# Kernel optimization log

Hardware: AMD Instinct MI355X
Metric: run time of the kernel (lower is better)

The kernel has to match this reference:

```python
import jax, jax.numpy as jnp
import numpy as np
import math


def _build_lookup(S):
    # Vectorized port of build_hierarchical_index_lookup_table (static, numpy).
    L = int(math.log2(S))
    total = 2 * S - 1
    max_valid = total - 2  # root is never a neighbor
    idx = np.full((S, L), -1, dtype=np.int32)
    cmask = np.zeros((S, L), dtype=bool)
    n = np.arange(S, dtype=np.int64)
    for lvl in range(L):
        if lvl == 0:
            nn = n ^ 1
            pair = n
        else:
            pair = n // 2 + S
            nn = pair ^ 1
        valid = nn <= max_valid
        idx[:, lvl] = np.where(valid, nn.astype(np.int32), idx[:, lvl])
        cmask[:, lvl] = np.where(valid, (pair < nn) & valid, cmask[:, lvl])
        n = nn
    return jnp.asarray(idx), jnp.asarray(cmask)


def _tree_kv(k, v, levels, scale):
    # Build parent nodes bottom-up. Parent K is the mean of its two children;
    # parent V is refined by the fused parent-self attention (build_parent_nodes):
    # 3-way softmax over [self, child0, child1] with eps 1e-9 in the denominator.
    K_parts, V_parts = [k], [v]
    Kc, Vc = k, v
    for _ in range(levels):
        Kc0, Kc1 = Kc[:, 0::2], Kc[:, 1::2]
        Vc0, Vc1 = Vc[:, 0::2], Vc[:, 1::2]
        Kp = 0.5 * (Kc0 + Kc1)
        Vp = 0.5 * (Vc0 + Vc1)
        s_self = jnp.einsum('bphd,bphd->bph', Kp, Kp) * scale
        s0 = jnp.einsum('bphd,bphd->bph', Kp, Kc0) * scale
        s1 = jnp.einsum('bphd,bphd->bph', Kp, Kc1) * scale
        m = jnp.maximum(s_self, jnp.maximum(s0, s1))
        e_self = jnp.exp(s_self - m)
        e0 = jnp.exp(s0 - m)
        e1 = jnp.exp(s1 - m)
        denom = e_self + e0 + e1 + 1e-9
        Vp = (e_self[..., None] * Vp + e0[..., None] * Vc0 + e1[..., None] * Vc1) / denom[..., None]
        K_parts.append(Kp)
        V_parts.append(Vp)
        Kc, Vc = Kp, Vp
    # Full tree: leaves first, then each parent level -> [B, 2S-1, H, D]
    return jnp.concatenate(K_parts, axis=1), jnp.concatenate(V_parts, axis=1)


def setup_inputs() -> dict:
    key = jax.random.key(0)
    kq, kk, kv = jax.random.split(key, 3)
    B, S, H, D = 4, 4096, 8, 64
    q = jax.random.normal(kq, (B, S, H, D), dtype=jnp.float32)
    k = jax.random.normal(kk, (B, S, H, D), dtype=jnp.float32)
    v = jax.random.normal(kv, (B, S, H, D), dtype=jnp.float32)
    return {'q': q, 'k': k, 'v': v}


def reference(q, k, v):
    B, S, H, D = q.shape
    L = int(math.log2(S))
    scale = 1.0 / math.sqrt(D)
    idx, cmask = _build_lookup(S)          # [S, L] int32, [S, L] bool
    Kf, Vf = _tree_kv(k, v, L, scale)      # [B, 2S-1, H, D]
    kc = Kf[:, idx]                        # [B, S, L, H, D] tree-indexed gather
    vc = Vf[:, idx]
    s_self = jnp.einsum('bshd,bshd->bsh', q, k) * scale
    s_cross = jnp.einsum('bshd,bslhd->bshl', q, kc) * scale
    s_cross = jnp.where(cmask[None, :, None, :], -jnp.inf, s_cross)
    m = jnp.maximum(s_self, jnp.max(s_cross, axis=-1))  # online-softmax max
    e_self = jnp.exp(s_self - m)
    e_cross = jnp.exp(s_cross - m[..., None])
    denom = e_self + jnp.sum(e_cross, axis=-1)
    out = (e_self[..., None] * v + jnp.einsum('bshl,bslhd->bshd', e_cross, vc)) / denom[..., None]
    return out
```

## Files before the change

kernel.cpp:

```cpp
#include <hip/hip_runtime.h>


#define S 4096
#define H 8
#define D 64
#define B 4
#define NBH 32
#define NHI 126
#define SCALE 0.125f

__device__ inline float red16(float x) {
    x += __shfl_xor(x, 1);
    x += __shfl_xor(x, 2);
    x += __shfl_xor(x, 4);
    x += __shfl_xor(x, 8);
    return x;
}

__device__ inline float dot4(const float4 a, const float4 b) {
    return a.x * b.x + a.y * b.y + a.z * b.z + a.w * b.w;
}

__device__ inline void combine(const float4 k0, const float4 k1,
                               const float4 v0, const float4 v1,
                               float4& kp, float4& vp) {
    kp.x = 0.5f * (k0.x + k1.x);
    kp.y = 0.5f * (k0.y + k1.y);
    kp.z = 0.5f * (k0.z + k1.z);
    kp.w = 0.5f * (k0.w + k1.w);
    float pss = red16(dot4(kp, kp)) * SCALE;
    float p0  = red16(dot4(kp, k0)) * SCALE;
    float p1  = red16(dot4(kp, k1)) * SCALE;
    float m  = fmaxf(pss, fmaxf(p0, p1));
    float es = __expf(pss - m), e0 = __expf(p0 - m), e1 = __expf(p1 - m);
    float inv = 1.0f / (es + e0 + e1 + 1e-9f);
    float h = 0.5f * es;
    vp.x = ((h + e0) * v0.x + (h + e1) * v1.x) * inv;
    vp.y = ((h + e0) * v0.y + (h + e1) * v1.y) * inv;
    vp.z = ((h + e0) * v0.z + (h + e1) * v1.z) * inv;
    vp.w = ((h + e0) * v0.w + (h + e1) * v1.w) * inv;
}

__global__ __launch_bounds__(256) void chunk_root(
    const float* __restrict__ k, const float* __restrict__ v,
    float* __restrict__ khi, float* __restrict__ vhi)
{
    __shared__ float lkA[32 * 64], lvA[32 * 64];
    __shared__ float lkB[16 * 64], lvB[16 * 64];
    const int t = threadIdx.x;
    const int sub = t & 15;
    const int pg = t >> 4;
    const int blk = blockIdx.x;
    const int c = blk & 63;
    const int bh = blk >> 6;
    const int b = bh >> 3, h = bh & 7;

#pragma unroll
    for (int r = 0; r < 2; ++r) {
        int j = pg + r * 16;
        int s0 = c * 64 + 2 * j;
        size_t a0 = ((((size_t)b * S + s0) * H + h) * D) + sub * 4;
        float4 k0 = *(const float4*)(k + a0);
        float4 k1 = *(const float4*)(k + a0 + H * D);
        float4 v0 = *(const float4*)(v + a0);
        float4 v1 = *(const float4*)(v + a0 + H * D);
        float4 kp, vp;
        combine(k0, k1, v0, v1, kp, vp);
        *(float4*)(lkA + j * 64 + sub * 4) = kp;
        *(float4*)(lvA + j * 64 + sub * 4) = vp;
    }
    __syncthreads();

    float *sk = lkA, *sv = lvA, *dk = lkB, *dv = lvB;
#pragma unroll
    for (int l = 2; l <= 6; ++l) {
        int np = 64 >> l;
        if (pg < np) {
            int j = pg;
            float4 k0 = *(const float4*)(sk + (2 * j) * 64 + sub * 4);
            float4 k1 = *(const float4*)(sk + (2 * j + 1) * 64 + sub * 4);
            float4 v0 = *(const float4*)(sv + (2 * j) * 64 + sub * 4);
            float4 v1 = *(const float4*)(sv + (2 * j + 1) * 64 + sub * 4);
            float4 kp, vp;
            combine(k0, k1, v0, v1, kp, vp);
            if (l < 6) {
                *(float4*)(dk + j * 64 + sub * 4) = kp;
                *(float4*)(dv + j * 64 + sub * 4) = vp;
            } else {
                size_t g = ((size_t)bh * NHI + c) * 64 + sub * 4;
                *(float4*)(khi + g) = kp;
                *(float4*)(vhi + g) = vp;
            }
        }
        __syncthreads();
        float* tp;
        tp = sk; sk = dk; dk = tp;
        tp = sv; sv = dv; dv = tp;
    }
}

__global__ __launch_bounds__(256) void build_hi(
    float* __restrict__ khi, float* __restrict__ vhi)
{
    __shared__ float lk[NHI * 64], lv[NHI * 64];
    const int t = threadIdx.x;
    const int sub = t & 15;
    const int pg = t >> 4;
    const int bh = blockIdx.x;
    size_t base = (size_t)bh * NHI * 64;

    for (int i = t; i < 1024; i += 256) {
        *(float4*)(lk + i * 4) = *(const float4*)(khi + base + i * 4);
        *(float4*)(lv + i * 4) = *(const float4*)(vhi + base + i * 4);
    }
    __syncthreads();

    int srcOff = 0, dstOff = 64, np = 32;
#pragma unroll
    for (int l = 7; l <= 11; ++l) {
        for (int j = pg; j < np; j += 16) {
            float4 k0 = *(const float4*)(lk + (srcOff + 2 * j) * 64 + sub * 4);
            float4 k1 = *(const float4*)(lk + (srcOff + 2 * j + 1) * 64 + sub * 4);
            float4 v0 = *(const float4*)(lv + (srcOff + 2 * j) * 64 + sub * 4);
            float4 v1 = *(const float4*)(lv + (srcOff + 2 * j + 1) * 64 + sub * 4);
            float4 kp, vp;
            combine(k0, k1, v0, v1, kp, vp);
            *(float4*)(lk + (dstOff + j) * 64 + sub * 4) = kp;
            *(float4*)(lv + (dstOff + j) * 64 + sub * 4) = vp;
            *(float4*)(khi + base + (size_t)(dstOff + j) * 64 + sub * 4) = kp;
            *(float4*)(vhi + base + (size_t)(dstOff + j) * 64 + sub * 4) = vp;
        }
        __syncthreads();
        srcOff = dstOff; dstOff += np; np >>= 1;
    }
}

__global__ __launch_bounds__(256) void attn_chunk(
    const float* __restrict__ q, const float* __restrict__ k,
    const float* __restrict__ v,
    const float* __restrict__ khi, const float* __restrict__ vhi,
    float* __restrict__ out)
{
    __shared__ float tk[62 * 64], tv[62 * 64];
    __shared__ float pk[6 * 64], pv[6 * 64];
    const int t = threadIdx.x;
    const int sub = t & 15;
    const int pg = t >> 4;
    const int blk = blockIdx.x;
    const int c = blk & 63;
    const int bh = blk >> 6;
    const int b = bh >> 3, h = bh & 7;

    if (pg < 12) {
        int lh = (pg >= 6) ? pg - 6 : pg;
        if ((c >> lh) & 1) {
            int off = 128 - (128 >> lh);
            int node = off + ((c >> lh) ^ 1);
            size_t a = ((size_t)bh * NHI + node) * 64 + sub * 4;
            if (pg < 6) *(float4*)(pk + lh * 64 + sub * 4) = *(const float4*)(khi + a);
            else        *(float4*)(pv + lh * 64 + sub * 4) = *(const float4*)(vhi + a);
        }
    }

#pragma unroll
    for (int r = 0; r < 2; ++r) {
        int j = pg + r * 16;
        int s0 = c * 64 + 2 * j;
        size_t a0 = ((((size_t)b * S + s0) * H + h) * D) + sub * 4;
        float4 k0 = *(const float4*)(k + a0);
        float4 k1 = *(const float4*)(k + a0 + H * D);
        float4 v0 = *(const float4*)(v + a0);
        float4 v1 = *(const float4*)(v + a0 + H * D);
        float4 kp, vp;
        combine(k0, k1, v0, v1, kp, vp);
        *(float4*)(tk + j * 64 + sub * 4) = kp;
        *(float4*)(tv + j * 64 + sub * 4) = vp;
    }
    __syncthreads();

    {
        int srcOff = 0, dstOff = 32, np = 16;
#pragma unroll
        for (int l = 2; l <= 5; ++l) {
            if (pg < np) {
                int j = pg;
                float4 k0 = *(const float4*)(tk + (srcOff + 2 * j) * 64 + sub * 4);
                float4 k1 = *(const float4*)(tk + (srcOff + 2 * j + 1) * 64 + sub * 4);
                float4 v0 = *(const float4*)(tv + (srcOff + 2 * j) * 64 + sub * 4);
                float4 v1 = *(const float4*)(tv + (srcOff + 2 * j + 1) * 64 + sub * 4);
                float4 kp, vp;
                combine(k0, k1, v0, v1, kp, vp);
                *(float4*)(tk + (dstOff + j) * 64 + sub * 4) = kp;
                *(float4*)(tv + (dstOff + j) * 64 + sub * 4) = vp;
            }
            __syncthreads();
            srcOff = dstOff; dstOff += np; np >>= 1;
        }
    }

#pragma unroll 1
    for (int r = 0; r < 4; ++r) {
        int sl = pg + r * 16;
        int s = c * 64 + sl;
        size_t qa = ((((size_t)b * S + s) * H + h) * D) + sub * 4;
        float4 q4 = *(const float4*)(q + qa);
        float4 k4 = *(const float4*)(k + qa);
        float4 v4 = *(const float4*)(v + qa);

        float ss = red16(dot4(q4, k4)) * SCALE;

        float sc[12];
        float4 vc0 = v4;
        const bool odd = (s & 1) != 0;
        if (odd) {
            float4 kc0 = *(const float4*)(k + qa - H * D);
            vc0 = *(const float4*)(v + qa - H * D);
            sc[0] = red16(dot4(q4, kc0)) * SCALE;
        } else {
            sc[0] = -1e38f;
        }
#pragma unroll
        for (int l = 1; l <= 5; ++l) {
            if ((s >> l) & 1) {
                int base = 64 - (64 >> (l - 1));
                int loc = base + (((s >> l) ^ 1) - (c << (6 - l)));
                float4 kc = *(const float4*)(tk + loc * 64 + sub * 4);
                sc[l] = red16(dot4(q4, kc)) * SCALE;
            } else sc[l] = -1e38f;
        }
#pragma unroll
        for (int l = 6; l <= 11; ++l) {
            if ((c >> (l - 6)) & 1) {
                float4 kc = *(const float4*)(pk + (l - 6) * 64 + sub * 4);
                sc[l] = red16(dot4(q4, kc)) * SCALE;
            } else sc[l] = -1e38f;
        }

        float m = ss;
#pragma unroll
        for (int l = 0; l < 12; ++l) m = fmaxf(m, sc[l]);

        float es = __expf(ss - m);
        float denom = es;
        float4 acc;
        acc.x = es * v4.x; acc.y = es * v4.y; acc.z = es * v4.z; acc.w = es * v4.w;

        if (odd) {
            float e = __expf(sc[0] - m);
            denom += e;
            acc.x += e * vc0.x; acc.y += e * vc0.y;
            acc.z += e * vc0.z; acc.w += e * vc0.w;
        }
#pragma unroll
        for (int l = 1; l <= 5; ++l) {
            if ((s >> l) & 1) {
                int base = 64 - (64 >> (l - 1));
                int loc = base + (((s >> l) ^ 1) - (c << (6 - l)));
                float4 vc = *(const float4*)(tv + loc * 64 + sub * 4);
                float e = __expf(sc[l] - m);
                denom += e;
                acc.x += e * vc.x; acc.y += e * vc.y;
                acc.z += e * vc.z; acc.w += e * vc.w;
            }
        }
#pragma unroll
        for (int l = 6; l <= 11; ++l) {
            if ((c >> (l - 6)) & 1) {
                float4 vc = *(const float4*)(pv + (l - 6) * 64 + sub * 4);
                float e = __expf(sc[l] - m);
                denom += e;
                acc.x += e * vc.x; acc.y += e * vc.y;
                acc.z += e * vc.z; acc.w += e * vc.w;
            }
        }
        float inv = 1.0f / denom;
        float4 o;
        o.x = acc.x * inv; o.y = acc.y * inv;
        o.z = acc.z * inv; o.w = acc.w * inv;
        *(float4*)(out + qa) = o;
    }
}

extern "C" void kernel_launch(void* const* d_in, const int* in_sizes, int n_in,
                              void* d_out, int out_size, void* d_ws, size_t ws_size,
                              hipStream_t stream) {
    const float* q = (const float*)d_in[0];
    const float* k = (const float*)d_in[1];
    const float* v = (const float*)d_in[2];
    float* outp = (float*)d_out;
    float* khi = (float*)d_ws;
    float* vhi = khi + (size_t)NBH * NHI * D;

    hipLaunchKernelGGL(chunk_root, dim3(NBH * 64), dim3(256), 0, stream,
                       k, v, khi, vhi);
    hipLaunchKernelGGL(build_hi, dim3(NBH), dim3(256), 0, stream, khi, vhi);
    hipLaunchKernelGGL(attn_chunk, dim3(NBH * 64), dim3(256), 0, stream,
                       q, k, v, khi, vhi, outp);
}
```

Before: 168.3 us.

## Fuse upper-tree build into attention kernel, recomputing high levels per block

Removes the separate build_hi kernel, which ran on only 32 blocks. Each attention block now loads all 64 chunk roots for its (b,h) into shared memory and rebuilds the upper tree levels in place, picking up the six sibling nodes it needs into registers. This drops one launch and a low-parallelism serial stage. In exchange each of the 2048 blocks repeats the upper-level reduction, with extra syncs and more shared memory. It also adds launch_bounds occupancy hints and partially unrolls the query loop.

```diff
diff --git a/kernel.cpp b/kernel.cpp
--- a/kernel.cpp
+++ b/kernel.cpp
@@ -6,7 +6,6 @@
 #define D 64
 #define B 4
 #define NBH 32
-#define NHI 126
 #define SCALE 0.125f
 
 __device__ inline float red16(float x) {
@@ -87,7 +86,7 @@
                 *(float4*)(dk + j * 64 + sub * 4) = kp;
                 *(float4*)(dv + j * 64 + sub * 4) = vp;
             } else {
-                size_t g = ((size_t)bh * NHI + c) * 64 + sub * 4;
+                size_t g = ((size_t)bh * 64 + c) * 64 + sub * 4;
                 *(float4*)(khi + g) = kp;
                 *(float4*)(vhi + g) = vp;
             }
@@ -99,50 +98,13 @@
     }
 }
 
-__global__ __launch_bounds__(256) void build_hi(
-    float* __restrict__ khi, float* __restrict__ vhi)
-{
-    __shared__ float lk[NHI * 64], lv[NHI * 64];
-    const int t = threadIdx.x;
-    const int sub = t & 15;
-    const int pg = t >> 4;
-    const int bh = blockIdx.x;
-    size_t base = (size_t)bh * NHI * 64;
-
-    for (int i = t; i < 1024; i += 256) {
-        *(float4*)(lk + i * 4) = *(const float4*)(khi + base + i * 4);
-        *(float4*)(lv + i * 4) = *(const float4*)(vhi + base + i * 4);
-    }
-    __syncthreads();
-
-    int srcOff = 0, dstOff = 64, np = 32;
-#pragma unroll
-    for (int l = 7; l <= 11; ++l) {
-        for (int j = pg; j < np; j += 16) {
-            float4 k0 = *(const float4*)(lk + (srcOff + 2 * j) * 64 + sub * 4);
-            float4 k1 = *(const float4*)(lk + (srcOff + 2 * j + 1) * 64 + sub * 4);
-            float4 v0 = *(const float4*)(lv + (srcOff + 2 * j) * 64 + sub * 4);
-            float4 v1 = *(const float4*)(lv + (srcOff + 2 * j + 1) * 64 + sub * 4);
-            float4 kp, vp;
-            combine(k0, k1, v0, v1, kp, vp);
-            *(float4*)(lk + (dstOff + j) * 64 + sub * 4) = kp;
-            *(float4*)(lv + (dstOff + j) * 64 + sub * 4) = vp;
-            *(float4*)(khi + base + (size_t)(dstOff + j) * 64 + sub * 4) = kp;
-            *(float4*)(vhi + base + (size_t)(dstOff + j) * 64 + sub * 4) = vp;
-        }
-        __syncthreads();
-        srcOff = dstOff; dstOff += np; np >>= 1;
-    }
-}
-
-__global__ __launch_bounds__(256) void attn_chunk(
+__global__ __launch_bounds__(256, 4) void attn_fused(
     const float* __restrict__ q, const float* __restrict__ k,
     const float* __restrict__ v,
     const float* __restrict__ khi, const float* __restrict__ vhi,
     float* __restrict__ out)
 {
-    __shared__ float tk[62 * 64], tv[62 * 64];
-    __shared__ float pk[6 * 64], pv[6 * 64];
+    __shared__ float rk[64 * 64], rv[64 * 64];
     const int t = threadIdx.x;
     const int sub = t & 15;
     const int pg = t >> 4;
@@ -151,15 +113,55 @@
     const int bh = blk >> 6;
     const int b = bh >> 3, h = bh & 7;
 
-    if (pg < 12) {
-        int lh = (pg >= 6) ? pg - 6 : pg;
-        if ((c >> lh) & 1) {
-            int off = 128 - (128 >> lh);
-            int node = off + ((c >> lh) ^ 1);
-            size_t a = ((size_t)bh * NHI + node) * 64 + sub * 4;
-            if (pg < 6) *(float4*)(pk + lh * 64 + sub * 4) = *(const float4*)(khi + a);
-            else        *(float4*)(pv + lh * 64 + sub * 4) = *(const float4*)(vhi + a);
-        }
+    {
+        size_t base = (size_t)bh * 64 * 64;
+        for (int i = t; i < 1024; i += 256) {
+            *(float4*)(rk + i * 4) = *(const float4*)(khi + base + i * 4);
+            *(float4*)(rv + i * 4) = *(const float4*)(vhi + base + i * 4);
+        }
+    }
+    __syncthreads();
+
+    float4 pkr[6], pvr[6];
+    pkr[0] = *(const float4*)(rk + (c ^ 1) * 64 + sub * 4);
+    pvr[0] = *(const float4*)(rv + (c ^ 1) * 64 + sub * 4);
+    __syncthreads();
+
+#pragma unroll
+    for (int tt = 1; tt <= 5; ++tt) {
+        int nc = 64 >> tt;
+        int half = 1 << (tt - 1);
+        if (tt == 1) {
+#pragma unroll
+            for (int r = 0; r < 2; ++r) {
+                int j = pg + r * 16;
+                int r0 = j << 1;
+                float4 k0 = *(const float4*)(rk + r0 * 64 + sub * 4);
+                float4 k1 = *(const float4*)(rk + (r0 + 1) * 64 + sub * 4);
+                float4 v0 = *(const float4*)(rv + r0 * 64 + sub * 4);
+                float4 v1 = *(const float4*)(rv + (r0 + 1) * 64 + sub * 4);
+                float4 kp, vp;
+                combine(k0, k1, v0, v1, kp, vp);
+                *(float4*)(rk + r0 * 64 + sub * 4) = kp;
+                *(float4*)(rv + r0 * 64 + sub * 4) = vp;
+            }
+        } else if (pg < nc) {
+            int r0 = pg << tt;
+            int r1 = r0 + half;
+            float4 k0 = *(const float4*)(rk + r0 * 64 + sub * 4);
+            float4 k1 = *(const float4*)(rk + r1 * 64 + sub * 4);
+            float4 v0 = *(const float4*)(rv + r0 * 64 + sub * 4);
+            float4 v1 = *(const float4*)(rv + r1 * 64 + sub * 4);
+            float4 kp, vp;
+            combine(k0, k1, v0, v1, kp, vp);
+            *(float4*)(rk + r0 * 64 + sub * 4) = kp;
+            *(float4*)(rv + r0 * 64 + sub * 4) = vp;
+        }
+        __syncthreads();
+        int prow = (((c >> tt) ^ 1)) << tt;
+        pkr[tt] = *(const float4*)(rk + prow * 64 + sub * 4);
+        pvr[tt] = *(const float4*)(rv + prow * 64 + sub * 4);
+        __syncthreads();
     }
 
 #pragma unroll
@@ -173,32 +175,31 @@
         float4 v1 = *(const float4*)(v + a0 + H * D);
         float4 kp, vp;
         combine(k0, k1, v0, v1, kp, vp);
-        *(float4*)(tk + j * 64 + sub * 4) = kp;
-        *(float4*)(tv + j * 64 + sub * 4) = vp;
-    }
-    __syncthreads();
-
+        *(float4*)(rk + j * 64 + sub * 4) = kp;
+        *(float4*)(rv + j * 64 + sub * 4) = vp;
+    }
+    __syncthreads();
     {
         int srcOff = 0, dstOff = 32, np = 16;
 #pragma unroll
         for (int l = 2; l <= 5; ++l) {
             if (pg < np) {
                 int j = pg;
-                float4 k0 = *(const float4*)(tk + (srcOff + 2 * j) * 64 + sub * 4);
-                float4 k1 = *(const float4*)(tk + (srcOff + 2 * j + 1) * 64 + sub * 4);
-                float4 v0 = *(const float4*)(tv + (srcOff + 2 * j) * 64 + sub * 4);
-                float4 v1 = *(const float4*)(tv + (srcOff + 2 * j + 1) * 64 + sub * 4);
+                float4 k0 = *(const float4*)(rk + (srcOff + 2 * j) * 64 + sub * 4);
+                float4 k1 = *(const float4*)(rk + (srcOff + 2 * j + 1) * 64 + sub * 4);
+                float4 v0 = *(const float4*)(rv + (srcOff + 2 * j) * 64 + sub * 4);
+                float4 v1 = *(const float4*)(rv + (srcOff + 2 * j + 1) * 64 + sub * 4);
                 float4 kp, vp;
                 combine(k0, k1, v0, v1, kp, vp);
-                *(float4*)(tk + (dstOff + j) * 64 + sub * 4) = kp;
-                *(float4*)(tv + (dstOff + j) * 64 + sub * 4) = vp;
+                *(float4*)(rk + (dstOff + j) * 64 + sub * 4) = kp;
+                *(float4*)(rv + (dstOff + j) * 64 + sub * 4) = vp;
             }
             __syncthreads();
             srcOff = dstOff; dstOff += np; np >>= 1;
         }
     }
 
-#pragma unroll 1
+#pragma unroll 2
     for (int r = 0; r < 4; ++r) {
         int sl = pg + r * 16;
         int s = c * 64 + sl;
@@ -224,15 +225,14 @@
             if ((s >> l) & 1) {
                 int base = 64 - (64 >> (l - 1));
                 int loc = base + (((s >> l) ^ 1) - (c << (6 - l)));
-                float4 kc = *(const float4*)(tk + loc * 64 + sub * 4);
+                float4 kc = *(const float4*)(rk + loc * 64 + sub * 4);
                 sc[l] = red16(dot4(q4, kc)) * SCALE;
             } else sc[l] = -1e38f;
         }
 #pragma unroll
         for (int l = 6; l <= 11; ++l) {
             if ((c >> (l - 6)) & 1) {
-                float4 kc = *(const float4*)(pk + (l - 6) * 64 + sub * 4);
-                sc[l] = red16(dot4(q4, kc)) * SCALE;
+                sc[l] = red16(dot4(q4, pkr[l - 6])) * SCALE;
             } else sc[l] = -1e38f;
         }
 
@@ -256,7 +256,7 @@
             if ((s >> l) & 1) {
                 int base = 64 - (64 >> (l - 1));
                 int loc = base + (((s >> l) ^ 1) - (c << (6 - l)));
-                float4 vc = *(const float4*)(tv + loc * 64 + sub * 4);
+                float4 vc = *(const float4*)(rv + loc * 64 + sub * 4);
                 float e = __expf(sc[l] - m);
                 denom += e;
                 acc.x += e * vc.x; acc.y += e * vc.y;
@@ -266,11 +266,10 @@
 #pragma unroll
         for (int l = 6; l <= 11; ++l) {
             if ((c >> (l - 6)) & 1) {
-                float4 vc = *(const float4*)(pv + (l - 6) * 64 + sub * 4);
                 float e = __expf(sc[l] - m);
                 denom += e;
-                acc.x += e * vc.x; acc.y += e * vc.y;
-                acc.z += e * vc.z; acc.w += e * vc.w;
+                acc.x += e * pvr[l - 6].x; acc.y += e * pvr[l - 6].y;
+                acc.z += e * pvr[l - 6].z; acc.w += e * pvr[l - 6].w;
             }
         }
         float inv = 1.0f / denom;
@@ -289,11 +288,10 @@
     const float* v = (const float*)d_in[2];
     float* outp = (float*)d_out;
     float* khi = (float*)d_ws;
-    float* vhi = khi + (size_t)NBH * NHI * D;
+    float* vhi = khi + (size_t)NBH * 64 * D;
 
     hipLaunchKernelGGL(chunk_root, dim3(NBH * 64), dim3(256), 0, stream,
                        k, v, khi, vhi);
-    hipLaunchKernelGGL(build_hi, dim3(NBH), dim3(256), 0, stream, khi, vhi);
-    hipLaunchKernelGGL(attn_chunk, dim3(NBH * 64), dim3(256), 0, stream,
+    hipLaunchKernelGGL(attn_fused, dim3(NBH * 64), dim3(256), 0, stream,
                        q, k, v, khi, vhi, outp);
 }
```

After: 169.6 us. About the same (+0.7%).

## Shrink attention chunks to 32 tokens and pad shared rows to avoid bank conflicts

Applied to the files above, without the earlier changes.

Reduces the per-block chunk in the attention kernel from 64 to 32 tokens and doubles the grid. Each chunk_root block now builds two 32-token subtrees in place. build_hi now processes 128 chunk roots over 6 levels. Shared-memory rows are padded to 68 floats to reduce LDS bank conflicts, and occupancy hints are added through launch_bounds. The aim is more parallelism and less per-block in-chunk tree work. The cost is more blocks that each redo the leaf-pair combine, plus a larger workspace.

```diff
diff --git a/kernel.cpp b/kernel.cpp
--- a/kernel.cpp
+++ b/kernel.cpp
@@ -6,8 +6,9 @@
 #define D 64
 #define B 4
 #define NBH 32
-#define NHI 126
+#define NHI 254
 #define SCALE 0.125f
+#define ROWF 68
 
 __device__ inline float red16(float x) {
     x += __shfl_xor(x, 1);
@@ -41,24 +42,27 @@
     vp.w = ((h + e0) * v0.w + (h + e1) * v1.w) * inv;
 }
 
-__global__ __launch_bounds__(256) void chunk_root(
+__global__ __launch_bounds__(256, 8) void chunk5(
     const float* __restrict__ k, const float* __restrict__ v,
     float* __restrict__ khi, float* __restrict__ vhi)
 {
-    __shared__ float lkA[32 * 64], lvA[32 * 64];
-    __shared__ float lkB[16 * 64], lvB[16 * 64];
+    __shared__ float lsk[32 * ROWF], lsv[32 * ROWF];
     const int t = threadIdx.x;
     const int sub = t & 15;
     const int pg = t >> 4;
     const int blk = blockIdx.x;
-    const int c = blk & 63;
+    const int pair = blk & 63;
     const int bh = blk >> 6;
     const int b = bh >> 3, h = bh & 7;
+    const int csel = pg >> 3;
+    const int jg = pg & 7;
+    const int c = pair * 2 + csel;
+    const int rowBase = csel * 16;
 
 #pragma unroll
     for (int r = 0; r < 2; ++r) {
-        int j = pg + r * 16;
-        int s0 = c * 64 + 2 * j;
+        int j = jg + r * 8;
+        int s0 = c * 32 + 2 * j;
         size_t a0 = ((((size_t)b * S + s0) * H + h) * D) + sub * 4;
         float4 k0 = *(const float4*)(k + a0);
         float4 k1 = *(const float4*)(k + a0 + H * D);
@@ -66,26 +70,26 @@
         float4 v1 = *(const float4*)(v + a0 + H * D);
         float4 kp, vp;
         combine(k0, k1, v0, v1, kp, vp);
-        *(float4*)(lkA + j * 64 + sub * 4) = kp;
-        *(float4*)(lvA + j * 64 + sub * 4) = vp;
-    }
-    __syncthreads();
-
-    float *sk = lkA, *sv = lvA, *dk = lkB, *dv = lvB;
-#pragma unroll
-    for (int l = 2; l <= 6; ++l) {
-        int np = 64 >> l;
-        if (pg < np) {
-            int j = pg;
-            float4 k0 = *(const float4*)(sk + (2 * j) * 64 + sub * 4);
-            float4 k1 = *(const float4*)(sk + (2 * j + 1) * 64 + sub * 4);
-            float4 v0 = *(const float4*)(sv + (2 * j) * 64 + sub * 4);
-            float4 v1 = *(const float4*)(sv + (2 * j + 1) * 64 + sub * 4);
+        *(float4*)(lsk + (rowBase + j) * ROWF + sub * 4) = kp;
+        *(float4*)(lsv + (rowBase + j) * ROWF + sub * 4) = vp;
+    }
+    __syncthreads();
+
+#pragma unroll
+    for (int tt = 1; tt <= 4; ++tt) {
+        int nodes = 16 >> tt;
+        for (int j = jg; j < nodes; j += 8) {
+            int r0 = rowBase + ((2 * j) << (tt - 1));
+            int r1 = rowBase + ((2 * j + 1) << (tt - 1));
+            float4 k0 = *(const float4*)(lsk + r0 * ROWF + sub * 4);
+            float4 k1 = *(const float4*)(lsk + r1 * ROWF + sub * 4);
+            float4 v0 = *(const float4*)(lsv + r0 * ROWF + sub * 4);
+            float4 v1 = *(const float4*)(lsv + r1 * ROWF + sub * 4);
             float4 kp, vp;
             combine(k0, k1, v0, v1, kp, vp);
-            if (l < 6) {
-                *(float4*)(dk + j * 64 + sub * 4) = kp;
-                *(float4*)(dv + j * 64 + sub * 4) = vp;
+            if (tt < 4) {
+                *(float4*)(lsk + (rowBase + (j << tt)) * ROWF + sub * 4) = kp;
+                *(float4*)(lsv + (rowBase + (j << tt)) * ROWF + sub * 4) = vp;
             } else {
                 size_t g = ((size_t)bh * NHI + c) * 64 + sub * 4;
                 *(float4*)(khi + g) = kp;
@@ -93,79 +97,81 @@
             }
         }
         __syncthreads();
-        float* tp;
-        tp = sk; sk = dk; dk = tp;
-        tp = sv; sv = dv; dv = tp;
     }
 }
 
 __global__ __launch_bounds__(256) void build_hi(
     float* __restrict__ khi, float* __restrict__ vhi)
 {
-    __shared__ float lk[NHI * 64], lv[NHI * 64];
+    __shared__ float lk[128 * ROWF], lv[128 * ROWF];
     const int t = threadIdx.x;
     const int sub = t & 15;
     const int pg = t >> 4;
     const int bh = blockIdx.x;
     size_t base = (size_t)bh * NHI * 64;
 
-    for (int i = t; i < 1024; i += 256) {
-        *(float4*)(lk + i * 4) = *(const float4*)(khi + base + i * 4);
-        *(float4*)(lv + i * 4) = *(const float4*)(vhi + base + i * 4);
-    }
-    __syncthreads();
-
-    int srcOff = 0, dstOff = 64, np = 32;
-#pragma unroll
-    for (int l = 7; l <= 11; ++l) {
-        for (int j = pg; j < np; j += 16) {
-            float4 k0 = *(const float4*)(lk + (srcOff + 2 * j) * 64 + sub * 4);
-            float4 k1 = *(const float4*)(lk + (srcOff + 2 * j + 1) * 64 + sub * 4);
-            float4 v0 = *(const float4*)(lv + (srcOff + 2 * j) * 64 + sub * 4);
-            float4 v1 = *(const float4*)(lv + (srcOff + 2 * j + 1) * 64 + sub * 4);
+    for (int i = t; i < 2048; i += 256) {
+        int row = i >> 4, s16 = i & 15;
+        *(float4*)(lk + row * ROWF + s16 * 4) = *(const float4*)(khi + base + i * 4);
+        *(float4*)(lv + row * ROWF + s16 * 4) = *(const float4*)(vhi + base + i * 4);
+    }
+    __syncthreads();
+
+#pragma unroll
+    for (int tt = 1; tt <= 6; ++tt) {
+        int nodes = 128 >> tt;
+        int off = 256 - (256 >> tt);
+        for (int j = pg; j < nodes; j += 16) {
+            int r0 = (2 * j) << (tt - 1);
+            int r1 = (2 * j + 1) << (tt - 1);
+            float4 k0 = *(const float4*)(lk + r0 * ROWF + sub * 4);
+            float4 k1 = *(const float4*)(lk + r1 * ROWF + sub * 4);
+            float4 v0 = *(const float4*)(lv + r0 * ROWF + sub * 4);
+            float4 v1 = *(const float4*)(lv + r1 * ROWF + sub * 4);
             float4 kp, vp;
             combine(k0, k1, v0, v1, kp, vp);
-            *(float4*)(lk + (dstOff + j) * 64 + sub * 4) = kp;
-            *(float4*)(lv + (dstOff + j) * 64 + sub * 4) = vp;
-            *(float4*)(khi + base + (size_t)(dstOff + j) * 64 + sub * 4) = kp;
-            *(float4*)(vhi + base + (size_t)(dstOff + j) * 64 + sub * 4) = vp;
+            *(float4*)(lk + (j << tt) * ROWF + sub * 4) = kp;
+            *(float4*)(lv + (j << tt) * ROWF + sub * 4) = vp;
+            size_t g = base + (size_t)(off + j) * 64 + sub * 4;
+            *(float4*)(khi + g) = kp;
+            *(float4*)(vhi + g) = vp;
         }
         __syncthreads();
-        srcOff = dstOff; dstOff += np; np >>= 1;
-    }
-}
-
-__global__ __launch_bounds__(256) void attn_chunk(
+    }
+}
+
+__global__ __launch_bounds__(256, 8) void attn32(
     const float* __restrict__ q, const float* __restrict__ k,
     const float* __restrict__ v,
     const float* __restrict__ khi, const float* __restrict__ vhi,
     float* __restrict__ out)
 {
-    __shared__ float tk[62 * 64], tv[62 * 64];
-    __shared__ float pk[6 * 64], pv[6 * 64];
+    __shared__ float tk[30 * ROWF], tv[30 * ROWF];
+    __shared__ float pk[7 * ROWF], pv[7 * ROWF];
     const int t = threadIdx.x;
     const int sub = t & 15;
     const int pg = t >> 4;
     const int blk = blockIdx.x;
-    const int c = blk & 63;
-    const int bh = blk >> 6;
+    const int c32 = blk & 127;
+    const int bh = blk >> 7;
     const int b = bh >> 3, h = bh & 7;
 
-    if (pg < 12) {
-        int lh = (pg >= 6) ? pg - 6 : pg;
-        if ((c >> lh) & 1) {
-            int off = 128 - (128 >> lh);
-            int node = off + ((c >> lh) ^ 1);
-            size_t a = ((size_t)bh * NHI + node) * 64 + sub * 4;
-            if (pg < 6) *(float4*)(pk + lh * 64 + sub * 4) = *(const float4*)(khi + a);
-            else        *(float4*)(pv + lh * 64 + sub * 4) = *(const float4*)(vhi + a);
-        }
-    }
-
-#pragma unroll
-    for (int r = 0; r < 2; ++r) {
-        int j = pg + r * 16;
-        int s0 = c * 64 + 2 * j;
+    {
+        int pl = (pg < 7) ? pg : pg - 8;
+        if (pl >= 0 && pl < 7 && pg != 7 && pg != 15) {
+            if ((c32 >> pl) & 1) {
+                int off = 256 - (256 >> pl);
+                int node = off + ((c32 >> pl) ^ 1);
+                size_t a = ((size_t)bh * NHI + node) * 64 + sub * 4;
+                if (pg < 7) *(float4*)(pk + pl * ROWF + sub * 4) = *(const float4*)(khi + a);
+                else        *(float4*)(pv + pl * ROWF + sub * 4) = *(const float4*)(vhi + a);
+            }
+        }
+    }
+
+    {
+        int j = pg;
+        int s0 = c32 * 32 + 2 * j;
         size_t a0 = ((((size_t)b * S + s0) * H + h) * D) + sub * 4;
         float4 k0 = *(const float4*)(k + a0);
         float4 k1 = *(const float4*)(k + a0 + H * D);
@@ -173,35 +179,51 @@
         float4 v1 = *(const float4*)(v + a0 + H * D);
         float4 kp, vp;
         combine(k0, k1, v0, v1, kp, vp);
-        *(float4*)(tk + j * 64 + sub * 4) = kp;
-        *(float4*)(tv + j * 64 + sub * 4) = vp;
-    }
-    __syncthreads();
-
-    {
-        int srcOff = 0, dstOff = 32, np = 16;
-#pragma unroll
-        for (int l = 2; l <= 5; ++l) {
-            if (pg < np) {
-                int j = pg;
-                float4 k0 = *(const float4*)(tk + (srcOff + 2 * j) * 64 + sub * 4);
-                float4 k1 = *(const float4*)(tk + (srcOff + 2 * j + 1) * 64 + sub * 4);
-                float4 v0 = *(const float4*)(tv + (srcOff + 2 * j) * 64 + sub * 4);
-                float4 v1 = *(const float4*)(tv + (srcOff + 2 * j + 1) * 64 + sub * 4);
-                float4 kp, vp;
-                combine(k0, k1, v0, v1, kp, vp);
-                *(float4*)(tk + (dstOff + j) * 64 + sub * 4) = kp;
-                *(float4*)(tv + (dstOff + j) * 64 + sub * 4) = vp;
-            }
-            __syncthreads();
-            srcOff = dstOff; dstOff += np; np >>= 1;
-        }
-    }
+        *(float4*)(tk + j * ROWF + sub * 4) = kp;
+        *(float4*)(tv + j * ROWF + sub * 4) = vp;
+    }
+    __syncthreads();
+    if (pg < 8) {
+        int j = pg;
+        float4 k0 = *(const float4*)(tk + (2 * j) * ROWF + sub * 4);
+        float4 k1 = *(const float4*)(tk + (2 * j + 1) * ROWF + sub * 4);
+        float4 v0 = *(const float4*)(tv + (2 * j) * ROWF + sub * 4);
+        float4 v1 = *(const float4*)(tv + (2 * j + 1) * ROWF + sub * 4);
+        float4 kp, vp;
+        combine(k0, k1, v0, v1, kp, vp);
+        *(float4*)(tk + (16 + j) * ROWF + sub * 4) = kp;
+        *(float4*)(tv + (16 + j) * ROWF + sub * 4) = vp;
+    }
+    __syncthreads();
+    if (pg < 4) {
+        int j = pg;
+        float4 k0 = *(const float4*)(tk + (16 + 2 * j) * ROWF + sub * 4);
+        float4 k1 = *(const float4*)(tk + (16 + 2 * j + 1) * ROWF + sub * 4);
+        float4 v0 = *(const float4*)(tv + (16 + 2 * j) * ROWF + sub * 4);
+        float4 v1 = *(const float4*)(tv + (16 + 2 * j + 1) * ROWF + sub * 4);
+        float4 kp, vp;
+        combine(k0, k1, v0, v1, kp, vp);
+        *(float4*)(tk + (24 + j) * ROWF + sub * 4) = kp;
+        *(float4*)(tv + (24 + j) * ROWF + sub * 4) = vp;
+    }
+    __syncthreads();
+    if (pg < 2) {
+        int j = pg;
+        float4 k0 = *(const float4*)(tk + (24 + 2 * j) * ROWF + sub * 4);
+        float4 k1 = *(const float4*)(tk + (24 + 2 * j + 1) * ROWF + sub * 4);
+        float4 v0 = *(const float4*)(tv + (24 + 2 * j) * ROWF + sub * 4);
+        float4 v1 = *(const float4*)(tv + (24 + 2 * j + 1) * ROWF + sub * 4);
+        float4 kp, vp;
+        combine(k0, k1, v0, v1, kp, vp);
+        *(float4*)(tk + (28 + j) * ROWF + sub * 4) = kp;
+        *(float4*)(tv + (28 + j) * ROWF + sub * 4) = vp;
+    }
+    __syncthreads();
 
 #pragma unroll 1
-    for (int r = 0; r < 4; ++r) {
-        int sl = pg + r * 16;
-        int s = c * 64 + sl;
+    for (int r = 0; r < 2; ++r) {
+        int sl = (pg >> 2) + (pg & 3) * 4 + r * 16;
+        int s = c32 * 32 + sl;
         size_t qa = ((((size_t)b * S + s) * H + h) * D) + sub * 4;
         float4 q4 = *(const float4*)(q + qa);
         float4 k4 = *(const float4*)(k + qa);
@@ -220,18 +242,18 @@
             sc[0] = -1e38f;
         }
 #pragma unroll
-        for (int l = 1; l <= 5; ++l) {
+        for (int l = 1; l <= 4; ++l) {
             if ((s >> l) & 1) {
-                int base = 64 - (64 >> (l - 1));
-                int loc = base + (((s >> l) ^ 1) - (c << (6 - l)));
-                float4 kc = *(const float4*)(tk + loc * 64 + sub * 4);
+                int base = 32 - (32 >> (l - 1));
+                int loc = base + (((s >> l) ^ 1) - (c32 << (5 - l)));
+                float4 kc = *(const float4*)(tk + loc * ROWF + sub * 4);
                 sc[l] = red16(dot4(q4, kc)) * SCALE;
             } else sc[l] = -1e38f;
         }
 #pragma unroll
-        for (int l = 6; l <= 11; ++l) {
-            if ((c >> (l - 6)) & 1) {
-                float4 kc = *(const float4*)(pk + (l - 6) * 64 + sub * 4);
+        for (int l = 5; l <= 11; ++l) {
+            if ((c32 >> (l - 5)) & 1) {
+                float4 kc = *(const float4*)(pk + (l - 5) * ROWF + sub * 4);
                 sc[l] = red16(dot4(q4, kc)) * SCALE;
             } else sc[l] = -1e38f;
         }
@@ -243,7 +265,8 @@
         float es = __expf(ss - m);
         float denom = es;
         float4 acc;
-        acc.x = es * v4.x; acc.y = es * v4.y; acc.z = es * v4.z; acc.w = es * v4.w;
+        acc.x = es * v4.x; acc.y = es * v4.y;
+        acc.z = es * v4.z; acc.w = es * v4.w;
 
         if (odd) {
             float e = __expf(sc[0] - m);
@@ -252,11 +275,11 @@
             acc.z += e * vc0.z; acc.w += e * vc0.w;
         }
 #pragma unroll
-        for (int l = 1; l <= 5; ++l) {
+        for (int l = 1; l <= 4; ++l) {
             if ((s >> l) & 1) {
-                int base = 64 - (64 >> (l - 1));
-                int loc = base + (((s >> l) ^ 1) - (c << (6 - l)));
-                float4 vc = *(const float4*)(tv + loc * 64 + sub * 4);
+                int base = 32 - (32 >> (l - 1));
+                int loc = base + (((s >> l) ^ 1) - (c32 << (5 - l)));
+                float4 vc = *(const float4*)(tv + loc * ROWF + sub * 4);
                 float e = __expf(sc[l] - m);
                 denom += e;
                 acc.x += e * vc.x; acc.y += e * vc.y;
@@ -264,9 +287,9 @@
             }
         }
 #pragma unroll
-        for (int l = 6; l <= 11; ++l) {
-            if ((c >> (l - 6)) & 1) {
-                float4 vc = *(const float4*)(pv + (l - 6) * 64 + sub * 4);
+        for (int l = 5; l <= 11; ++l) {
+            if ((c32 >> (l - 5)) & 1) {
+                float4 vc = *(const float4*)(pv + (l - 5) * ROWF + sub * 4);
                 float e = __expf(sc[l] - m);
                 denom += e;
                 acc.x += e * vc.x; acc.y += e * vc.y;
@@ -291,9 +314,9 @@
     float* khi = (float*)d_ws;
     float* vhi = khi + (size_t)NBH * NHI * D;
 
-    hipLaunchKernelGGL(chunk_root, dim3(NBH * 64), dim3(256), 0, stream,
+    hipLaunchKernelGGL(chunk5, dim3(NBH * 64), dim3(256), 0, stream,
                        k, v, khi, vhi);
     hipLaunchKernelGGL(build_hi, dim3(NBH), dim3(256), 0, stream, khi, vhi);
-    hipLaunchKernelGGL(attn_chunk, dim3(NBH * 64), dim3(256), 0, stream,
+    hipLaunchKernelGGL(attn32, dim3(NBH * 128), dim3(256), 0, stream,
                        q, k, v, khi, vhi, outp);
 }
```

Result: no change. 166.9 us (-0.9%).
